# Kernel optimization log

Measured on AMD Instinct MI355X. Metric: run time of the kernel, lower is better.

The kernel has to match this reference:

```python
import jax, jax.numpy as jnp
import numpy as np

EPS = 1e-5


def _conv(x, w, pad):
    return jax.lax.conv_general_dilated(
        x, w, (1, 1), [(pad, pad), (pad, pad)],
        dimension_numbers=('NCHW', 'OIHW', 'NCHW'))


def _reflect_pad1(x):
    return jnp.pad(x, ((0, 0), (0, 0), (1, 1), (1, 1)), mode='reflect')


def _instance_norm(x):
    m = x.mean((2, 3), keepdims=True)
    v = x.var((2, 3), keepdims=True)  # biased, as torch InstanceNorm2d
    return (x - m) * jax.lax.rsqrt(v + EPS)


def _batch_norm(x, g, b):
    m = x.mean((0, 2, 3), keepdims=True)
    v = x.var((0, 2, 3), keepdims=True)
    return (x - m) * jax.lax.rsqrt(v + EPS) * g.reshape(1, -1, 1, 1) + b.reshape(1, -1, 1, 1)


def _dct_ortho(x):
    # DCT-II with 'ortho' norm along last axis (same math as torch_dct.dct)
    N = x.shape[-1]
    v = jnp.concatenate([x[..., ::2], x[..., 1::2][..., ::-1]], axis=-1)
    Vc = jnp.fft.fft(v)
    k = jnp.arange(N) * (np.pi / (2.0 * N))
    V = Vc.real * jnp.cos(k) + Vc.imag * jnp.sin(k)
    scale = jnp.full((N,), 1.0 / np.sqrt(N / 2.0), dtype=x.dtype).at[0].set(1.0 / np.sqrt(float(N)))
    return V * scale


def _idct_ortho(X):
    # DCT-III (inverse of ortho DCT-II) along last axis (same math as torch_dct.idct)
    N = X.shape[-1]
    scale = jnp.full((N,), np.sqrt(N / 2.0), dtype=X.dtype).at[0].set(np.sqrt(float(N)))
    Xv = X * scale
    k = jnp.arange(N) * (np.pi / (2.0 * N))
    Wr, Wi = jnp.cos(k), jnp.sin(k)
    Vti = jnp.concatenate([jnp.zeros_like(Xv[..., :1]), -Xv[..., ::-1][..., :-1]], axis=-1)
    V = (Xv * Wr - Vti * Wi) + 1j * (Xv * Wi + Vti * Wr)
    v = jnp.fft.ifft(V).real
    out = jnp.zeros_like(v)
    out = out.at[..., ::2].set(v[..., : (N + 1) // 2])
    out = out.at[..., 1::2].set(v[..., ::-1][..., : N // 2])
    return out


def setup_inputs() -> dict:
    key = jax.random.key(0)
    ks = iter(jax.random.split(key, 32))
    B, C, H, W = 4, 128, 128, 128
    R = C // 16  # SFOM ratio
    d = {'x': jax.random.normal(next(ks), (B, C, H, W), jnp.float32)}
    d['conv1_w'] = jax.random.normal(next(ks), (C, C, 3, 3), jnp.float32) * 0.05
    d['conv1_b'] = jnp.zeros((C,), jnp.float32)
    d['conv2_w'] = jax.random.normal(next(ks), (C, C, 3, 3), jnp.float32) * 0.05
    d['conv2_b'] = jnp.zeros((C,), jnp.float32)
    # SFOM spectral attention MLP (torch Linear weights: [out, in])
    d['sa_w1'] = jax.random.normal(next(ks), (R, C), jnp.float32) * 0.1
    d['sa_w2'] = jax.random.normal(next(ks), (C, R), jnp.float32) * 0.1
    # SPEM dynamic-conv pyramid: 128->32->64->128->128->64->32, k=7
    chans = [(C, 32), (32, 64), (64, 128), (128, 128), (128, 64), (64, 32)]
    for i, (ci, co) in enumerate(chans, 1):
        d[f'dw{i}'] = jax.random.normal(next(ks), (co, ci, 7, 7), jnp.float32) * (0.05 / np.sqrt(ci))
        d[f'bg{i}'] = jnp.ones((co,), jnp.float32)
        d[f'bb{i}'] = jnp.zeros((co,), jnp.float32)
    d['spem_cw'] = jax.random.normal(next(ks), (1, 32, 1, 1), jnp.float32) * 0.1
    d['spem_cb'] = jnp.zeros((1,), jnp.float32)
    return d


def reference(x, conv1_w, conv1_b, conv2_w, conv2_b, sa_w1, sa_w2,
              dw1, bg1, bb1, dw2, bg2, bb2, dw3, bg3, bb3,
              dw4, bg4, bb4, dw5, bg5, bb5, dw6, bg6, bb6,
              spem_cw, spem_cb):
    # conv1: reflect pad 1 + conv(padding=1) -> spatial grows by 2
    out = _conv(_reflect_pad1(x), conv1_w, 1) + conv1_b.reshape(1, -1, 1, 1)
    out = jax.nn.relu(_instance_norm(out))
    out = _conv(_reflect_pad1(out), conv2_w, 1) + conv2_b.reshape(1, -1, 1, 1)
    out = _instance_norm(out)
    # SFOM channel attention via DCT gating
    B, C, H, W = out.shape
    dctx = _dct_ortho(out.reshape(B, C, H * W)).reshape(B, C, H, W)
    m = dctx.mean((2, 3))  # [B, C]
    gate = jax.nn.sigmoid(jax.nn.relu(m @ sa_w1.T) @ sa_w2.T)  # [B, C]
    idctx = _idct_ortho((dctx * gate[:, :, None, None]).reshape(B, C, H * W)).reshape(B, C, H, W)
    out = jax.nn.sigmoid((out + idctx) * 0.5) * out
    # SPEM spatial attention; DynamicConv2d repeats one shared filter per sample,
    # which is mathematically identical to a plain conv with that filter.
    h = out
    for w_, g_, b_ in ((dw1, bg1, bb1), (dw2, bg2, bb2), (dw3, bg3, bb3),
                       (dw4, bg4, bb4), (dw5, bg5, bb5), (dw6, bg6, bb6)):
        h = jax.nn.relu(_batch_norm(_conv(h, w_, 3), g_, b_))
    sa = jax.nn.sigmoid(_conv(h, spem_cw, 0) + spem_cb.reshape(1, -1, 1, 1))
    return sa * out
```

## Files before the change

### kernel.cpp

```cpp
#include <hip/hip_runtime.h>
#include <math.h>

#define B_    4
#define HW1   (130*130)
#define HW2   (132*132)
#define NBUF  ((size_t)B_*128*HW2)
#define EPS_  1e-5f
#define PI_   3.14159265358979f

typedef _Float16 half8 __attribute__((ext_vector_type(8)));
typedef _Float16 half4_ __attribute__((ext_vector_type(4)));
typedef float    float4_ __attribute__((ext_vector_type(4)));

struct WPackArgs {
  const float* src[8];
  _Float16*    dst[8];
  int cout[8], cin[8], kk[8];
  int off[9];
};
__global__ void wpack_all(WPackArgs p) {
  int idx = blockIdx.x * blockDim.x + threadIdx.x;
  if (idx >= p.off[8]) return;
  int s = 0;
  while (idx >= p.off[s + 1]) ++s;
  int i = idx - p.off[s];
  int Cin = p.cin[s], K = p.kk[s];
  int KK = K * K, COG = p.cout[s] / 16;
  int j    = i & 7;
  int lane = (i >> 3) & 63;
  int rest = i >> 9;
  int g    = rest % COG; rest /= COG;
  int tap  = rest % KK;
  int cc   = rest / KK;
  int n = lane & 15, q = lane >> 4;
  int co = g * 16 + n;
  int ci = cc * 32 + q * 8 + j;
  p.dst[s][i] = (_Float16)p.src[s][((size_t)co * Cin + ci) * KK + tap];
}

__global__ void to_nhwc(const float* __restrict__ in, _Float16* __restrict__ out,
                        int C, int HW) {
  __shared__ float t[32][65];
  int b = blockIdx.z, c0 = blockIdx.y * 32, p0 = blockIdx.x * 64;
  int tid = threadIdx.x;
  for (int i = 0; i < 8; ++i) {
    int e = i * 256 + tid; int cl = e >> 6, pl = e & 63;
    int p = p0 + pl;
    float v = 0.f;
    if (p < HW) v = in[((size_t)b * C + c0 + cl) * HW + p];
    t[cl][pl] = v;
  }
  __syncthreads();
  for (int i = 0; i < 8; ++i) {
    int e = i * 256 + tid; int pl = e >> 5, cl = e & 31;
    int p = p0 + pl;
    if (p < HW) out[((size_t)b * HW + p) * C + c0 + cl] = (_Float16)t[cl][pl];
  }
}

__global__ void zerok(float* p, int n) {
  int i = blockIdx.x * blockDim.x + threadIdx.x;
  if (i < n) p[i] = 0.f;
}

template<int CIN, int COUT, int K, int HIN, int HOUT, bool REFLECT, int AFF, bool RELU, bool POB>
__global__ __launch_bounds__(256, 2) void conv_mfma(
    const _Float16* __restrict__ act, const _Float16* __restrict__ wp,
    const float* __restrict__ sums_in, const float* __restrict__ gam,
    const float* __restrict__ bet, float invn, float* __restrict__ sums_out,
    _Float16* __restrict__ out) {
  constexpr int NWC = (COUT >= 64) ? 2 : 1;
  constexpr int WCO = COUT / NWC;
  constexpr int MR  = WCO / 16;
  constexpr int NWR = 4 / NWC;
  constexpr int ROWS = NWR * 4;
  constexpr int PADc = (K - 1) / 2;
  constexpr int IR = ROWS + K - 1;
  constexpr int XW = 16 + K - 1;
  constexpr int CH = IR * 4 * XW;
  constexpr int COG = COUT / 16;
  constexpr int KK = K * K;
  constexpr int XT = (HOUT + 15) / 16;
  constexpr int NSLAB = CIN / 32;
  constexpr int NST = (CH + 255) / 256;

  __shared__ half8 smem[2][CH];
  __shared__ float2 snorm[CIN];
  __shared__ float bsum[COUT * 2];

  const int xt = blockIdx.x % XT, yt = blockIdx.x / XT;
  const int x0 = xt * 16, y0 = yt * ROWS;
  const int b = blockIdx.z;
  const int tid = threadIdx.x;
  const int lane = tid & 63, w = tid >> 6;
  const int wc = (NWC == 2) ? (w & 1) : 0;
  const int wr = (NWC == 2) ? (w >> 1) : w;
  const int n = lane & 15, q = lane >> 4;

  if (AFF) {
    if (tid < CIN) {
      int idx = (AFF == 1 ? b * CIN : 0) + tid;
      float m  = sums_in[idx * 2] * invn;
      float vr = sums_in[idx * 2 + 1] * invn - m * m;
      float sc = rsqrtf(vr + EPS_);
      if (AFF == 2) sc *= gam[tid];
      float sh = (AFF == 2 ? bet[tid] : 0.f) - m * sc;
      snorm[tid] = make_float2(sc, sh);
    }
  }
  if (tid < COUT) { bsum[tid * 2] = 0.f; bsum[tid * 2 + 1] = 0.f; }

  float4_ acc[MR][4];
#pragma unroll
  for (int mi = 0; mi < MR; ++mi)
#pragma unroll
    for (int ni = 0; ni < 4; ++ni)
#pragma unroll
      for (int j = 0; j < 4; ++j) acc[mi][ni][j] = 0.f;

  const _Float16* actb = act + (size_t)b * HIN * HIN * CIN;

  int sidx[NST];
  int soff[NST];
#pragma unroll
  for (int i = 0; i < NST; ++i) {
    int e = tid + i * 256;
    sidx[i] = -1; soff[i] = -1;
    if (e < CH) {
      int qq = e & 3, rx = e >> 2;
      int row = rx / XW, lx = rx % XW;
      int ty = y0 + row - PADc;
      int tx = x0 + lx - PADc;
      bool ok; int iy, ix;
      if (REFLECT) {
        ok = (ty >= 0 && ty < HIN + 2 && tx >= 0 && tx < HIN + 2);
        iy = (ty == 0) ? 1 : (ty == HIN + 1 ? HIN - 2 : ty - 1);
        ix = (tx == 0) ? 1 : (tx == HIN + 1 ? HIN - 2 : tx - 1);
      } else {
        ok = (ty >= 0 && ty < HIN && tx >= 0 && tx < HIN);
        iy = ty; ix = tx;
      }
      sidx[i] = (row * 4 + qq) * XW + lx;
      if (ok) soff[i] = (iy * HIN + ix) * CIN + qq * 8;
    }
  }

  auto ldS = [&](int cc, half8* v) {
#pragma unroll
    for (int i = 0; i < NST; ++i) {
#pragma unroll
      for (int j = 0; j < 8; ++j) v[i][j] = (_Float16)0.f;
      if (soff[i] >= 0) v[i] = *(const half8*)(actb + soff[i] + cc * 32);
    }
  };
  auto wrS = [&](int cc, int buf, half8* v) {
    float nsc[8], nsh[8];
    if (AFF) {
      int cb2 = cc * 32 + (tid & 3) * 8;
#pragma unroll
      for (int j = 0; j < 8; ++j) { float2 t = snorm[cb2 + j]; nsc[j] = t.x; nsh[j] = t.y; }
    }
#pragma unroll
    for (int i = 0; i < NST; ++i) {
      if (sidx[i] >= 0) {
        half8 t = v[i];
        if (AFF && soff[i] >= 0) {
#pragma unroll
          for (int j = 0; j < 8; ++j) {
            float f = (float)t[j] * nsc[j] + nsh[j];
            if (RELU) f = fmaxf(f, 0.f);
            t[j] = (_Float16)f;
          }
        }
        smem[buf][sidx[i]] = t;
      }
    }
  };

  half8 stg[NST];
  ldS(0, stg);
  __syncthreads();
  wrS(0, 0, stg);

  for (int cc = 0; cc < NSLAB; ++cc) {
    const int cur = cc & 1;
    if (cc + 1 < NSLAB) ldS(cc + 1, stg);
    asm volatile("s_waitcnt lgkmcnt(0)" ::: "memory");
    __builtin_amdgcn_s_barrier();

    auto ldA = [&](int tap, half8* a) {
#pragma unroll
      for (int mi = 0; mi < MR; ++mi) {
        int g = wc * MR + mi;
        a[mi] = *(const half8*)(wp + (((size_t)(cc * KK + tap) * COG + g) * 64 + lane) * 8);
      }
    };
    auto ldB = [&](int tap, half8* c) {
      int ky = tap / K, kx = tap % K;
#pragma unroll
      for (int ni = 0; ni < 4; ++ni)
        c[ni] = smem[cur][((wr * 4 + ni + ky) * 4 + q) * XW + n + kx];
    };
    auto domf = [&](half8* a, half8* c) {
#pragma unroll
      for (int mi = 0; mi < MR; ++mi)
#pragma unroll
        for (int ni = 0; ni < 4; ++ni)
          acc[mi][ni] = __builtin_amdgcn_mfma_f32_16x16x32_f16(a[mi], c[ni], acc[mi][ni], 0, 0, 0);
    };
    half8 a0[MR], a1[MR], c0[4], c1[4];
    ldA(0, a0); ldB(0, c0);
    for (int tap = 0; tap + 1 < KK; tap += 2) {
      ldA(tap + 1, a1); ldB(tap + 1, c1);
      domf(a0, c0);
      ldA(tap + 2, a0); ldB(tap + 2, c0);
      domf(a1, c1);
    }
    domf(a0, c0);

    if (cc + 1 < NSLAB) wrS(cc + 1, cur ^ 1, stg);
  }

  const bool xv = (x0 + n) < HOUT;
#pragma unroll
  for (int mi = 0; mi < MR; ++mi) {
#pragma unroll
    for (int j = 0; j < 4; ++j) {
      float s = 0.f, s2 = 0.f;
#pragma unroll
      for (int ni = 0; ni < 4; ++ni) {
        int y = y0 + wr * 4 + ni;
        float f = acc[mi][ni][j];
        bool v = xv && (y < HOUT);
        s  += v ? f : 0.f;
        s2 += v ? f * f : 0.f;
      }
#pragma unroll
      for (int off = 1; off < 16; off <<= 1) {
        s  += __shfl_xor(s,  off, 64);
        s2 += __shfl_xor(s2, off, 64);
      }
      if (n == 0) {
        int co = wc * WCO + mi * 16 + q * 4 + j;
        atomicAdd(&bsum[co * 2],     s);
        atomicAdd(&bsum[co * 2 + 1], s2);
      }
    }
  }
  _Float16* outb = out + (size_t)b * HOUT * HOUT * COUT;
#pragma unroll
  for (int mi = 0; mi < MR; ++mi) {
#pragma unroll
    for (int ni = 0; ni < 4; ++ni) {
      int y = y0 + wr * 4 + ni, x = x0 + n;
      if (y < HOUT && x < HOUT) {
        int co = wc * WCO + mi * 16 + q * 4;
        half4_ h;
#pragma unroll
        for (int j = 0; j < 4; ++j) h[j] = (_Float16)acc[mi][ni][j];
        *(half4_*)(outb + ((size_t)y * HOUT + x) * COUT + co) = h;
      }
    }
  }
  __syncthreads();
  if (tid < COUT) {
    int idx = (POB ? b * COUT : 0) + tid;
    atomicAdd(&sums_out[idx * 2],     bsum[tid * 2]);
    atomicAdd(&sums_out[idx * 2 + 1], bsum[tid * 2 + 1]);
  }
}

__global__ void wdctk(float* __restrict__ wd, int N) {
  int i = blockIdx.x * blockDim.x + threadIdx.x;
  if (i >= N) return;
  float Nf = (float)N;
  float c2 = 0.5f * sqrtf(2.f / Nf);
  float a  = sqrtf(1.f / Nf) - c2;
  float phi = PI_ / (4.f * Nf) * (2.f * i + 1.f);
  float cot = cosf(phi) / sinf(phi);
  wd[i] = a + ((i & 1) ? -c2 : c2) * cot;
}

__global__ void mdctk(const _Float16* __restrict__ x, const float* __restrict__ wd,
                      const float* __restrict__ sums2, float invn,
                      float* __restrict__ md, int HW) {
  int b = blockIdx.z, tid = threadIdx.x;
  int c = tid & 127, pr = tid >> 7;
  int slab = blockIdx.x, nsl = gridDim.x;
  float m  = sums2[(b * 128 + c) * 2] * invn;
  float sc = rsqrtf(sums2[(b * 128 + c) * 2 + 1] * invn - m * m + EPS_);
  float sh = -m * sc;
  const _Float16* xb = x + (size_t)b * HW * 128;
  float s = 0.f;
  for (int p = slab * 2 + pr; p < HW; p += nsl * 2)
    s += ((float)xb[(size_t)p * 128 + c] * sc + sh) * wd[p];
  __shared__ float l1[256];
  l1[tid] = s;
  __syncthreads();
  if (tid < 128) atomicAdd(&md[b * 128 + c], l1[tid] + l1[tid + 128]);
}

__global__ void gatek(const float* __restrict__ md, const float* __restrict__ w1,
                      const float* __restrict__ w2, float* __restrict__ gate) {
  __shared__ float t1[4][8];
  int tid = threadIdx.x;
  const float invN = 1.f / (float)HW2;
  if (tid < 32) {
    int b = tid >> 3, r = tid & 7;
    float s = 0.f;
    for (int c = 0; c < 128; ++c) s += md[b * 128 + c] * invN * w1[r * 128 + c];
    t1[b][r] = fmaxf(s, 0.f);
  }
  __syncthreads();
  int b = tid >> 7, c = tid & 127;
  float s = 0.f;
#pragma unroll
  for (int r = 0; r < 8; ++r) s += t1[b][r] * w2[c * 8 + r];
  gate[tid] = 1.f / (1.f + expf(-s));
}

__global__ void sfomk(const _Float16* __restrict__ x, const float* __restrict__ sums2,
                      float invn, const float* __restrict__ gate,
                      _Float16* __restrict__ o, int HW) {
  size_t idx = (size_t)blockIdx.x * blockDim.x + threadIdx.x;
  size_t tot = (size_t)4 * HW * 16;
  if (idx >= tot) return;
  int cg = (int)(idx % 16);
  size_t bp = idx / 16;
  int b = (int)(bp / HW);
  half8 v = *(const half8*)(x + bp * 128 + cg * 8);
  half8 r;
#pragma unroll
  for (int j = 0; j < 8; ++j) {
    int c = cg * 8 + j;
    float m  = sums2[(b * 128 + c) * 2] * invn;
    float sc = rsqrtf(sums2[(b * 128 + c) * 2 + 1] * invn - m * m + EPS_);
    float f = (float)v[j] * sc - m * sc;
    float g = gate[b * 128 + c];
    float s = 1.f / (1.f + expf(-(f * (1.f + g) * 0.5f)));
    r[j] = (_Float16)(s * f);
  }
  *(half8*)(o + bp * 128 + cg * 8) = r;
}

__global__ void sak(const _Float16* __restrict__ h, const float* __restrict__ sums6,
                    float invn, const float* __restrict__ gam, const float* __restrict__ bet,
                    const float* __restrict__ cw, const float* __restrict__ cb,
                    float* __restrict__ sa) {
  __shared__ float ssc[32], ssh[32];
  int tid = threadIdx.x;
  if (tid < 32) {
    float m  = sums6[tid * 2] * invn;
    float sc = rsqrtf(sums6[tid * 2 + 1] * invn - m * m + EPS_) * gam[tid];
    ssc[tid] = sc;
    ssh[tid] = bet[tid] - m * sc;
  }
  __syncthreads();
  int idx = blockIdx.x * blockDim.x + tid;
  if (idx >= 4 * HW2) return;
  const _Float16* p = h + (size_t)idx * 32;
  float s = cb[0];
#pragma unroll
  for (int c = 0; c < 32; ++c)
    s += fmaxf((float)p[c] * ssc[c] + ssh[c], 0.f) * cw[c];
  sa[idx] = 1.f / (1.f + expf(-s));
}

__global__ void finalt(const _Float16* __restrict__ o, const float* __restrict__ sa,
                       float* __restrict__ out) {
  __shared__ float t[32][65];
  int b = blockIdx.z, c0 = blockIdx.y * 32, p0 = blockIdx.x * 64;
  int tid = threadIdx.x;
  for (int i = 0; i < 8; ++i) {
    int e = i * 256 + tid; int pl = e >> 5, cl = e & 31;
    int p = p0 + pl;
    if (p < HW2)
      t[cl][pl] = (float)o[((size_t)b * HW2 + p) * 128 + c0 + cl] * sa[b * HW2 + p];
  }
  __syncthreads();
  for (int i = 0; i < 8; ++i) {
    int e = i * 256 + tid; int cl = e >> 6, pl = e & 63;
    int p = p0 + pl;
    if (p < HW2)
      out[((size_t)b * 128 + c0 + cl) * HW2 + p] = t[cl][pl];
  }
}

extern "C" void kernel_launch(void* const* d_in, const int* in_sizes, int n_in,
                              void* d_out, int out_size, void* d_ws, size_t ws_size,
                              hipStream_t stream) {
  const float* x     = (const float*)d_in[0];
  const float* c1w   = (const float*)d_in[1];
  const float* c2w   = (const float*)d_in[3];
  const float* sa_w1 = (const float*)d_in[5];
  const float* sa_w2 = (const float*)d_in[6];
  const float* dw[6] = {(const float*)d_in[7],  (const float*)d_in[10], (const float*)d_in[13],
                        (const float*)d_in[16], (const float*)d_in[19], (const float*)d_in[22]};
  const float* bg[6] = {(const float*)d_in[8],  (const float*)d_in[11], (const float*)d_in[14],
                        (const float*)d_in[17], (const float*)d_in[20], (const float*)d_in[23]};
  const float* bb[6] = {(const float*)d_in[9],  (const float*)d_in[12], (const float*)d_in[15],
                        (const float*)d_in[18], (const float*)d_in[21], (const float*)d_in[24]};
  const float* cw    = (const float*)d_in[25];
  const float* cb    = (const float*)d_in[26];
  float* out = (float*)d_out;

  char* wsp = (char*)d_ws;
  auto alloc = [&](size_t bytes) { char* p = wsp; wsp += (bytes + 255) & ~(size_t)255; return p; };
  _Float16* B0 = (_Float16*)alloc(NBUF * 2);
  _Float16* B1 = (_Float16*)alloc(NBUF * 2);
  _Float16* B2 = (_Float16*)alloc(NBUF * 2);
  _Float16* B3 = (_Float16*)alloc(NBUF * 2);
  _Float16* wp_c1 = (_Float16*)alloc((size_t)128 * 128 * 9 * 2);
  _Float16* wp_c2 = (_Float16*)alloc((size_t)128 * 128 * 9 * 2);
  const int sci[6] = {128, 32, 64, 128, 128, 64};
  const int sco[6] = {32, 64, 128, 128, 64, 32};
  _Float16* wp_d[6];
  for (int i = 0; i < 6; ++i) wp_d[i] = (_Float16*)alloc((size_t)sco[i] * sci[i] * 49 * 2);
  float* SUMS = (float*)alloc(8704 * 4);
  float* s_c1 = SUMS;
  float* s_c2 = SUMS + 1024;
  float* s_l[6];
  for (int i = 0; i < 6; ++i) s_l[i] = SUMS + 2048 + i * 1024;
  float* md   = SUMS + 8192;
  float* gate = (float*)alloc(512 * 4);
  float* wd   = (float*)alloc((size_t)HW2 * 4);
  float* sa   = (float*)alloc((size_t)4 * HW2 * 4);

  {
    WPackArgs p;
    p.src[0] = c1w; p.dst[0] = wp_c1; p.cout[0] = 128; p.cin[0] = 128; p.kk[0] = 3;
    p.src[1] = c2w; p.dst[1] = wp_c2; p.cout[1] = 128; p.cin[1] = 128; p.kk[1] = 3;
    for (int i = 0; i < 6; ++i) {
      p.src[2 + i] = dw[i]; p.dst[2 + i] = wp_d[i];
      p.cout[2 + i] = sco[i]; p.cin[2 + i] = sci[i]; p.kk[2 + i] = 7;
    }
    p.off[0] = 0;
    for (int i = 0; i < 8; ++i) p.off[i + 1] = p.off[i] + p.cout[i] * p.cin[i] * p.kk[i] * p.kk[i];
    wpack_all<<<(p.off[8] + 255) / 256, 256, 0, stream>>>(p);
  }

  to_nhwc<<<dim3(16384 / 64, 4, 4), 256, 0, stream>>>(x, B0, 128, 16384);
  zerok<<<34, 256, 0, stream>>>(SUMS, 8704);

  const float i1 = 1.f / (float)HW1, i2 = 1.f / (float)HW2, ib = 1.f / (4.f * HW2);

  conv_mfma<128, 128, 3, 128, 130, true, 0, false, true><<<dim3(9 * 17, 1, 4), 256, 0, stream>>>(
      B0, wp_c1, nullptr, nullptr, nullptr, 0.f, s_c1, B1);
  conv_mfma<128, 128, 3, 130, 132, true, 1, true, true><<<dim3(9 * 17, 1, 4), 256, 0, stream>>>(
      B1, wp_c2, s_c1, nullptr, nullptr, i1, s_c2, B2);

  wdctk<<<(HW2 + 255) / 256, 256, 0, stream>>>(wd, HW2);
  mdctk<<<dim3(128, 1, 4), 256, 0, stream>>>(B2, wd, s_c2, i2, md, HW2);
  gatek<<<1, 512, 0, stream>>>(md, sa_w1, sa_w2, gate);
  { size_t tot = (size_t)4 * HW2 * 16;
    sfomk<<<(int)((tot + 255) / 256), 256, 0, stream>>>(B2, s_c2, i2, gate, B3, HW2); }

  conv_mfma<128, 32, 7, 132, 132, false, 0, false, false><<<dim3(9 * 9, 1, 4), 256, 0, stream>>>(
      B3, wp_d[0], nullptr, nullptr, nullptr, 0.f, s_l[0], B0);
  conv_mfma<32, 64, 7, 132, 132, false, 2, true, false><<<dim3(9 * 17, 1, 4), 256, 0, stream>>>(
      B0, wp_d[1], s_l[0], bg[0], bb[0], ib, s_l[1], B1);
  conv_mfma<64, 128, 7, 132, 132, false, 2, true, false><<<dim3(9 * 17, 1, 4), 256, 0, stream>>>(
      B1, wp_d[2], s_l[1], bg[1], bb[1], ib, s_l[2], B0);
  conv_mfma<128, 128, 7, 132, 132, false, 2, true, false><<<dim3(9 * 17, 1, 4), 256, 0, stream>>>(
      B0, wp_d[3], s_l[2], bg[2], bb[2], ib, s_l[3], B1);
  conv_mfma<128, 64, 7, 132, 132, false, 2, true, false><<<dim3(9 * 17, 1, 4), 256, 0, stream>>>(
      B1, wp_d[4], s_l[3], bg[3], bb[3], ib, s_l[4], B0);
  conv_mfma<64, 32, 7, 132, 132, false, 2, true, false><<<dim3(9 * 9, 1, 4), 256, 0, stream>>>(
      B0, wp_d[5], s_l[4], bg[4], bb[4], ib, s_l[5], B1);

  sak<<<(4 * HW2 + 255) / 256, 256, 0, stream>>>(B1, s_l[5], ib, bg[5], bb[5], cw, cb, sa);
  finalt<<<dim3((HW2 + 63) / 64, 4, 4), 256, 0, stream>>>(B3, sa, out);
}
```

Measured before the change: 736.6 us.

## Use 32x32x16 MFMA tiles for the 7x7 SPEM convolutions

```diff
diff --git a/kernel.cpp b/kernel.cpp
--- a/kernel.cpp
+++ b/kernel.cpp
@@ -11,11 +11,12 @@
 typedef _Float16 half8 __attribute__((ext_vector_type(8)));
 typedef _Float16 half4_ __attribute__((ext_vector_type(4)));
 typedef float    float4_ __attribute__((ext_vector_type(4)));
+typedef float    f32x16 __attribute__((ext_vector_type(16)));
 
 struct WPackArgs {
   const float* src[8];
   _Float16*    dst[8];
-  int cout[8], cin[8], kk[8];
+  int cout[8], cin[8], kk[8], m32[8];
   int off[9];
 };
 __global__ void wpack_all(WPackArgs p) {
@@ -25,17 +26,29 @@
   while (idx >= p.off[s + 1]) ++s;
   int i = idx - p.off[s];
   int Cin = p.cin[s], K = p.kk[s];
-  int KK = K * K, COG = p.cout[s] / 16;
+  int KK = K * K;
   int j    = i & 7;
   int lane = (i >> 3) & 63;
   int rest = i >> 9;
-  int g    = rest % COG; rest /= COG;
-  int tap  = rest % KK;
-  int cc   = rest / KK;
-  int n = lane & 15, q = lane >> 4;
-  int co = g * 16 + n;
-  int ci = cc * 32 + q * 8 + j;
-  p.dst[s][i] = (_Float16)p.src[s][((size_t)co * Cin + ci) * KK + tap];
+  int co, ci;
+  if (p.m32[s]) {
+    int NMT = p.cout[s] / 32;
+    int kh  = rest & 1; rest >>= 1;
+    int mtg = rest % NMT; rest /= NMT;
+    int tap = rest % KK;
+    int cc  = rest / KK;
+    co = mtg * 32 + (lane & 31);
+    ci = cc * 32 + kh * 16 + (lane >> 5) * 8 + j;
+    p.dst[s][i] = (_Float16)p.src[s][((size_t)co * Cin + ci) * KK + tap];
+  } else {
+    int COG = p.cout[s] / 16;
+    int g   = rest % COG; rest /= COG;
+    int tap = rest % KK;
+    int cc  = rest / KK;
+    co = g * 16 + (lane & 15);
+    ci = cc * 32 + (lane >> 4) * 8 + j;
+    p.dst[s][i] = (_Float16)p.src[s][((size_t)co * Cin + ci) * KK + tap];
+  }
 }
 
 __global__ void to_nhwc(const float* __restrict__ in, _Float16* __restrict__ out,
@@ -72,6 +85,8 @@
   constexpr int NWC = (COUT >= 64) ? 2 : 1;
   constexpr int WCO = COUT / NWC;
   constexpr int MR  = WCO / 16;
+  constexpr int MT  = WCO / 32;
+  constexpr int NMT = COUT / 32;
   constexpr int NWR = 4 / NWC;
   constexpr int ROWS = NWR * 4;
   constexpr int PADc = (K - 1) / 2;
@@ -111,12 +126,22 @@
   if (tid < COUT) { bsum[tid * 2] = 0.f; bsum[tid * 2 + 1] = 0.f; }
 
   float4_ acc[MR][4];
-#pragma unroll
-  for (int mi = 0; mi < MR; ++mi)
-#pragma unroll
-    for (int ni = 0; ni < 4; ++ni)
-#pragma unroll
-      for (int j = 0; j < 4; ++j) acc[mi][ni][j] = 0.f;
+  f32x16  acc32[MT][2];
+  if constexpr (K >= 5) {
+#pragma unroll
+    for (int mt = 0; mt < MT; ++mt)
+#pragma unroll
+      for (int rp = 0; rp < 2; ++rp)
+#pragma unroll
+        for (int j = 0; j < 16; ++j) acc32[mt][rp][j] = 0.f;
+  } else {
+#pragma unroll
+    for (int mi = 0; mi < MR; ++mi)
+#pragma unroll
+      for (int ni = 0; ni < 4; ++ni)
+#pragma unroll
+        for (int j = 0; j < 4; ++j) acc[mi][ni][j] = 0.f;
+  }
 
   const _Float16* actb = act + (size_t)b * HIN * HIN * CIN;
 
@@ -188,77 +213,165 @@
     asm volatile("s_waitcnt lgkmcnt(0)" ::: "memory");
     __builtin_amdgcn_s_barrier();
 
-    auto ldA = [&](int tap, half8* a) {
-#pragma unroll
-      for (int mi = 0; mi < MR; ++mi) {
-        int g = wc * MR + mi;
-        a[mi] = *(const half8*)(wp + (((size_t)(cc * KK + tap) * COG + g) * 64 + lane) * 8);
-      }
-    };
-    auto ldB = [&](int tap, half8* c) {
-      int ky = tap / K, kx = tap % K;
-#pragma unroll
-      for (int ni = 0; ni < 4; ++ni)
-        c[ni] = smem[cur][((wr * 4 + ni + ky) * 4 + q) * XW + n + kx];
-    };
-    auto domf = [&](half8* a, half8* c) {
-#pragma unroll
-      for (int mi = 0; mi < MR; ++mi)
+    if constexpr (K >= 5) {
+      const int dy = q & 1, qh = q >> 1;
+      auto ldA = [&](int tap, half8* a) {
+#pragma unroll
+        for (int mt = 0; mt < MT; ++mt)
+#pragma unroll
+          for (int kh = 0; kh < 2; ++kh)
+            a[mt * 2 + kh] = *(const half8*)(
+                wp + ((((size_t)(cc * KK + tap)) * NMT + (wc * MT + mt)) * 2 + kh) * 512
+                   + (size_t)lane * 8);
+      };
+      auto ldB = [&](int tap, half8* c) {
+        int ky = tap / K, kx = tap % K;
+#pragma unroll
+        for (int rp = 0; rp < 2; ++rp)
+#pragma unroll
+          for (int kh = 0; kh < 2; ++kh)
+            c[rp * 2 + kh] =
+                smem[cur][((wr * 4 + rp * 2 + dy + ky) * 4 + kh * 2 + qh) * XW + n + kx];
+      };
+      auto domf = [&](half8* a, half8* c) {
+#pragma unroll
+        for (int mt = 0; mt < MT; ++mt)
+#pragma unroll
+          for (int rp = 0; rp < 2; ++rp) {
+            acc32[mt][rp] = __builtin_amdgcn_mfma_f32_32x32x16_f16(
+                a[mt * 2 + 0], c[rp * 2 + 0], acc32[mt][rp], 0, 0, 0);
+            acc32[mt][rp] = __builtin_amdgcn_mfma_f32_32x32x16_f16(
+                a[mt * 2 + 1], c[rp * 2 + 1], acc32[mt][rp], 0, 0, 0);
+          }
+      };
+      half8 a0[MT * 2], a1[MT * 2], c0[4], c1[4];
+      ldA(0, a0); ldB(0, c0);
+      for (int tap = 0; tap + 1 < KK; tap += 2) {
+        ldA(tap + 1, a1); ldB(tap + 1, c1);
+        domf(a0, c0);
+        ldA(tap + 2, a0); ldB(tap + 2, c0);
+        domf(a1, c1);
+      }
+      domf(a0, c0);
+    } else {
+      auto ldA = [&](int tap, half8* a) {
+#pragma unroll
+        for (int mi = 0; mi < MR; ++mi) {
+          int g = wc * MR + mi;
+          a[mi] = *(const half8*)(wp + (((size_t)(cc * KK + tap) * COG + g) * 64 + lane) * 8);
+        }
+      };
+      auto ldB = [&](int tap, half8* c) {
+        int ky = tap / K, kx = tap % K;
 #pragma unroll
         for (int ni = 0; ni < 4; ++ni)
-          acc[mi][ni] = __builtin_amdgcn_mfma_f32_16x16x32_f16(a[mi], c[ni], acc[mi][ni], 0, 0, 0);
-    };
-    half8 a0[MR], a1[MR], c0[4], c1[4];
-    ldA(0, a0); ldB(0, c0);
-    for (int tap = 0; tap + 1 < KK; tap += 2) {
-      ldA(tap + 1, a1); ldB(tap + 1, c1);
+          c[ni] = smem[cur][((wr * 4 + ni + ky) * 4 + q) * XW + n + kx];
+      };
+      auto domf = [&](half8* a, half8* c) {
+#pragma unroll
+        for (int mi = 0; mi < MR; ++mi)
+#pragma unroll
+          for (int ni = 0; ni < 4; ++ni)
+            acc[mi][ni] = __builtin_amdgcn_mfma_f32_16x16x32_f16(a[mi], c[ni], acc[mi][ni], 0, 0, 0);
+      };
+      half8 a0[MR], a1[MR], c0[4], c1[4];
+      ldA(0, a0); ldB(0, c0);
+      for (int tap = 0; tap + 1 < KK; tap += 2) {
+        ldA(tap + 1, a1); ldB(tap + 1, c1);
+        domf(a0, c0);
+        ldA(tap + 2, a0); ldB(tap + 2, c0);
+        domf(a1, c1);
+      }
       domf(a0, c0);
-      ldA(tap + 2, a0); ldB(tap + 2, c0);
-      domf(a1, c1);
-    }
-    domf(a0, c0);
+    }
 
     if (cc + 1 < NSLAB) wrS(cc + 1, cur ^ 1, stg);
   }
 
+  _Float16* outb = out + (size_t)b * HOUT * HOUT * COUT;
   const bool xv = (x0 + n) < HOUT;
-#pragma unroll
-  for (int mi = 0; mi < MR; ++mi) {
-#pragma unroll
-    for (int j = 0; j < 4; ++j) {
-      float s = 0.f, s2 = 0.f;
+
+  if constexpr (K >= 5) {
+    const int dy = q & 1, qh = q >> 1;
+#pragma unroll
+    for (int mt = 0; mt < MT; ++mt) {
+#pragma unroll
+      for (int g = 0; g < 4; ++g)
+#pragma unroll
+        for (int jj = 0; jj < 4; ++jj) {
+          float s = 0.f, s2 = 0.f;
+#pragma unroll
+          for (int rp = 0; rp < 2; ++rp) {
+            int y = y0 + wr * 4 + rp * 2 + dy;
+            float f = acc32[mt][rp][g * 4 + jj];
+            bool v = xv && (y < HOUT);
+            s  += v ? f : 0.f;
+            s2 += v ? f * f : 0.f;
+          }
+#pragma unroll
+          for (int off = 1; off < 32; off <<= 1) {
+            s  += __shfl_xor(s,  off, 64);
+            s2 += __shfl_xor(s2, off, 64);
+          }
+          if ((lane & 31) == 0) {
+            int co = wc * WCO + mt * 32 + g * 8 + qh * 4 + jj;
+            atomicAdd(&bsum[co * 2],     s);
+            atomicAdd(&bsum[co * 2 + 1], s2);
+          }
+        }
+#pragma unroll
+      for (int rp = 0; rp < 2; ++rp) {
+        int y = y0 + wr * 4 + rp * 2 + dy, x = x0 + n;
+        if (y < HOUT && x < HOUT) {
+#pragma unroll
+          for (int g = 0; g < 4; ++g) {
+            int co = wc * WCO + mt * 32 + g * 8 + qh * 4;
+            half4_ h;
+#pragma unroll
+            for (int jj = 0; jj < 4; ++jj) h[jj] = (_Float16)acc32[mt][rp][g * 4 + jj];
+            *(half4_*)(outb + ((size_t)y * HOUT + x) * COUT + co) = h;
+          }
+        }
+      }
+    }
+  } else {
+#pragma unroll
+    for (int mi = 0; mi < MR; ++mi) {
+#pragma unroll
+      for (int j = 0; j < 4; ++j) {
+        float s = 0.f, s2 = 0.f;
+#pragma unroll
+        for (int ni = 0; ni < 4; ++ni) {
+          int y = y0 + wr * 4 + ni;
+          float f = acc[mi][ni][j];
+          bool v = xv && (y < HOUT);
+          s  += v ? f : 0.f;
+          s2 += v ? f * f : 0.f;
+        }
+#pragma unroll
+        for (int off = 1; off < 16; off <<= 1) {
+          s  += __shfl_xor(s,  off, 64);
+          s2 += __shfl_xor(s2, off, 64);
+        }
+        if (n == 0) {
+          int co = wc * WCO + mi * 16 + q * 4 + j;
+          atomicAdd(&bsum[co * 2],     s);
+          atomicAdd(&bsum[co * 2 + 1], s2);
+        }
+      }
+    }
+#pragma unroll
+    for (int mi = 0; mi < MR; ++mi) {
 #pragma unroll
       for (int ni = 0; ni < 4; ++ni) {
-        int y = y0 + wr * 4 + ni;
-        float f = acc[mi][ni][j];
-        bool v = xv && (y < HOUT);
-        s  += v ? f : 0.f;
-        s2 += v ? f * f : 0.f;
-      }
-#pragma unroll
-      for (int off = 1; off < 16; off <<= 1) {
-        s  += __shfl_xor(s,  off, 64);
-        s2 += __shfl_xor(s2, off, 64);
-      }
-      if (n == 0) {
-        int co = wc * WCO + mi * 16 + q * 4 + j;
-        atomicAdd(&bsum[co * 2],     s);
-        atomicAdd(&bsum[co * 2 + 1], s2);
-      }
-    }
-  }
-  _Float16* outb = out + (size_t)b * HOUT * HOUT * COUT;
-#pragma unroll
-  for (int mi = 0; mi < MR; ++mi) {
-#pragma unroll
-    for (int ni = 0; ni < 4; ++ni) {
-      int y = y0 + wr * 4 + ni, x = x0 + n;
-      if (y < HOUT && x < HOUT) {
-        int co = wc * WCO + mi * 16 + q * 4;
-        half4_ h;
-#pragma unroll
-        for (int j = 0; j < 4; ++j) h[j] = (_Float16)acc[mi][ni][j];
-        *(half4_*)(outb + ((size_t)y * HOUT + x) * COUT + co) = h;
+        int y = y0 + wr * 4 + ni, x = x0 + n;
+        if (y < HOUT && x < HOUT) {
+          int co = wc * WCO + mi * 16 + q * 4;
+          half4_ h;
+#pragma unroll
+          for (int j = 0; j < 4; ++j) h[j] = (_Float16)acc[mi][ni][j];
+          *(half4_*)(outb + ((size_t)y * HOUT + x) * COUT + co) = h;
+        }
       }
     }
   }
@@ -428,11 +541,11 @@
 
   {
     WPackArgs p;
-    p.src[0] = c1w; p.dst[0] = wp_c1; p.cout[0] = 128; p.cin[0] = 128; p.kk[0] = 3;
-    p.src[1] = c2w; p.dst[1] = wp_c2; p.cout[1] = 128; p.cin[1] = 128; p.kk[1] = 3;
+    p.src[0] = c1w; p.dst[0] = wp_c1; p.cout[0] = 128; p.cin[0] = 128; p.kk[0] = 3; p.m32[0] = 0;
+    p.src[1] = c2w; p.dst[1] = wp_c2; p.cout[1] = 128; p.cin[1] = 128; p.kk[1] = 3; p.m32[1] = 0;
     for (int i = 0; i < 6; ++i) {
       p.src[2 + i] = dw[i]; p.dst[2 + i] = wp_d[i];
-      p.cout[2 + i] = sco[i]; p.cin[2 + i] = sci[i]; p.kk[2 + i] = 7;
+      p.cout[2 + i] = sco[i]; p.cin[2 + i] = sci[i]; p.kk[2 + i] = 7; p.m32[2 + i] = 1;
     }
     p.off[0] = 0;
     for (int i = 0; i < 8; ++i) p.off[i + 1] = p.off[i] + p.cout[i] * p.cin[i] * p.kk[i] * p.kk[i];
```

Result: slower. 766.5 us (+4.1%).
